# Kernel optimization log

Hardware: AMD Instinct MI355X
Metric: run time of the kernel (lower is better)

## Reference

```python
import jax, jax.numpy as jnp
import numpy as np

CURVS = (-1.0, 0.0, 1.0, -0.5)
N, E, B = 50000, 800000, 128
IN, HID, OUT, GHID = 128, 128, 128, 32
K = len(CURVS)
TAU_MIN, TAU_MAX = 0.05, 10.0
EPS = 1e-15


def _vnorm(x):
    return jnp.maximum(jnp.linalg.norm(x, axis=-1, keepdims=True), EPS)


def tan_k(x, k):
    if k > 0:
        sk = np.sqrt(k)
        return jnp.tan(x * sk) / sk
    if k < 0:
        sk = np.sqrt(-k)
        return jnp.tanh(x * sk) / sk
    return x


def artan_k(x, k):
    if k > 0:
        sk = np.sqrt(k)
        return jnp.arctan(x * sk) / sk
    if k < 0:
        sk = np.sqrt(-k)
        return jnp.arctanh(jnp.clip(x * sk, -1.0 + 1e-7, 1.0 - 1e-7)) / sk
    return x


def project(x, k):
    # clip inside Poincare ball for k<0; identity otherwise (geoopt Stereographic.projx)
    if k < 0:
        maxn = (1.0 - 1e-5) / np.sqrt(-k)
        n = _vnorm(x)
        return jnp.where(n > maxn, x * (maxn / n), x)
    return x


def expmap0(u, k):
    n = _vnorm(u)
    return project(tan_k(n, k) * u / n, k)


def logmap0(y, k):
    n = _vnorm(y)
    return artan_k(n, k) * y / n


def mobius_add(x, y, k):
    x2 = jnp.sum(x * x, -1, keepdims=True)
    y2 = jnp.sum(y * y, -1, keepdims=True)
    xy = jnp.sum(x * y, -1, keepdims=True)
    num = (1.0 - 2.0 * k * xy - k * y2) * x + (1.0 + k * x2) * y
    den = jnp.maximum(1.0 - 2.0 * k * xy + k * k * x2 * y2, 1e-15)
    return project(num / den, k)


def mobius_matvec(W, x, k):
    mx = x @ W.T
    if k == 0:
        return mx
    xn = _vnorm(x)
    mxn = _vnorm(mx)
    res = tan_k(mxn / xn * artan_k(xn, k), k) * mx / mxn
    res = jnp.where(jnp.sum(jnp.abs(mx), -1, keepdims=True) == 0.0, 0.0, res)
    return project(res, k)


def dist(x, y, k):
    return 2.0 * artan_k(_vnorm(mobius_add(-x, y, k)), k)[..., 0]


def setup_inputs():
    key = jax.random.key(0)
    ks = jax.random.split(key, 12)
    x = jax.random.normal(ks[0], (N, IN), jnp.float32)
    edge_index = jax.random.randint(ks[1], (2, E), 0, N)
    batch = jnp.sort(jax.random.randint(ks[2], (N,), 0, B))
    s1 = float(np.sqrt(2.0 / (IN + HID)))
    s2 = float(np.sqrt(2.0 / (HID + OUT)))
    sg1 = float(np.sqrt(2.0 / (IN + GHID)))
    sg2 = float(np.sqrt(2.0 / (GHID + OUT)))
    raw0 = float(np.log(np.expm1(1.0 - TAU_MIN)))
    return {
        "x": x,
        "edge_index": edge_index,
        "batch": batch,
        "expert_w1": jax.random.normal(ks[3], (K, HID, IN), jnp.float32) * s1,
        "expert_b1": jnp.zeros((K, HID), jnp.float32),
        "expert_w2": jax.random.normal(ks[4], (K, OUT, HID), jnp.float32) * s2,
        "expert_b2": jnp.zeros((K, OUT), jnp.float32),
        "gate_w1": jax.random.normal(ks[5], (GHID, IN), jnp.float32) * sg1,
        "gate_b1": jnp.zeros((GHID,), jnp.float32),
        "gate_w2": jax.random.normal(ks[6], (OUT, GHID), jnp.float32) * sg2,
        "gate_b2": jnp.zeros((OUT,), jnp.float32),
        "gate_u": jax.random.normal(ks[7], (K, OUT), jnp.float32) * 0.02,
        "tau_raw": jnp.full((K,), raw0, jnp.float32),
    }


def _graph_norm(edge_index):
    loops = jnp.arange(N)
    row = jnp.concatenate([edge_index[0], loops])
    col = jnp.concatenate([edge_index[1], loops])
    deg = jax.ops.segment_sum(jnp.ones(E + N, jnp.float32), col, num_segments=N)
    dinv = deg ** -0.5  # deg >= 1 due to self loops
    return row, col, dinv[row] * dinv[col]


def _kappa_conv(xm, W, b, row, col, enorm, k):
    h = mobius_matvec(W, xm, k)
    bias_pt = expmap0(b[None, :], k)  # proju at origin is identity
    h = mobius_add(h, bias_pt, k)
    t = logmap0(h, k)  # [N, out]
    agg = jax.ops.segment_sum(enorm[:, None] * t[row], col, num_segments=N)
    return expmap0(agg, k)


def reference(x, edge_index, batch, expert_w1, expert_b1, expert_w2, expert_b2,
              gate_w1, gate_b1, gate_w2, gate_b2, gate_u, tau_raw):
    x = x.astype(jnp.float32)
    row, col, enorm = _graph_norm(edge_index)
    counts = jnp.maximum(
        jax.ops.segment_sum(jnp.ones(N, jnp.float32), batch, num_segments=B), 1.0)[:, None]

    # --- Riemannian experts ---
    embs = []
    for i, kv in enumerate(CURVS):
        xm = expmap0(x, kv)  # manifold init (proju at origin = identity)
        xm = _kappa_conv(xm, expert_w1[i], expert_b1[i], row, col, enorm, kv)
        xm = _kappa_conv(xm, expert_w2[i], expert_b2[i], row, col, enorm, kv)
        z = logmap0(xm, kv)
        embs.append(jax.ops.segment_sum(z, batch, num_segments=B) / counts)
    features = jnp.concatenate(embs, axis=-1)  # [B, K*OUT]

    # --- Euclidean gating encoder (GCN) ---
    def gcn(h, W, b):
        m = (h @ W.T)
        out = jax.ops.segment_sum(enorm[:, None] * m[row], col, num_segments=N) + b
        return jax.nn.relu(out)

    g = gcn(x, gate_w1, gate_b1)
    g = gcn(g, gate_w2, gate_b2)
    hgate = jax.ops.segment_sum(g, batch, num_segments=B) / counts  # [B, OUT]

    # --- Geometric distance gate ---
    tau = jnp.clip(jax.nn.softplus(tau_raw) + TAU_MIN, TAU_MIN, TAU_MAX)
    dists = []
    for i, kv in enumerate(CURVS):
        zk = expmap0(hgate, kv)
        yk = expmap0(gate_u[i][None, :], kv)
        dists.append(dist(zk, yk, kv))
    dists = jnp.stack(dists, axis=-1)  # [B, K]
    weights = jax.nn.softmax(-dists / tau[None, :], axis=-1)

    scaled = features * jnp.repeat(weights, OUT, axis=1)
    return scaled, weights, dists, tau
```

## Files before the change

### kernel.cpp

```cpp
#include <hip/hip_runtime.h>
#include <math.h>

#define NN 50000
#define EE 800000
#define ETOT (EE + NN)
#define BB 128
#define DIM 128
#define GHID 32
#define CHUNK 128
#define NCHUNK ((ETOT + CHUNK - 1) / CHUNK)
#define SCB 196

typedef _Float16 f16;
typedef _Float16 f16x2 __attribute__((ext_vector_type(2)));
typedef _Float16 f16x8 __attribute__((ext_vector_type(8)));
typedef float f32x4 __attribute__((ext_vector_type(4)));

struct CurvPack {
  float k[4], sk[4], mx[4], thr2[4];
};

__device__ __forceinline__ float wsum64(float v) {
#pragma unroll
  for (int m = 32; m; m >>= 1) v += __shfl_xor(v, m, 64);
  return v;
}

__device__ __forceinline__ float tan_k_d(float x, float kv, float sk) {
  if (kv > 0.f) return tanf(x * sk) / sk;
  if (kv < 0.f) return tanhf(x * sk) / sk;
  return x;
}

__device__ __forceinline__ float artan_k_d(float x, float kv, float sk) {
  if (kv > 0.f) return atanf(x * sk) / sk;
  if (kv < 0.f) {
    float t = x * sk;
    t = fminf(fmaxf(t, -1.f + 1e-7f), 1.f - 1e-7f);
    return atanhf(t) / sk;
  }
  return x;
}

__device__ __forceinline__ float proj_scale_d(float n, float kv, float maxn) {
  if (kv < 0.f && n > maxn) return maxn / n;
  return 1.f;
}

__global__ void k_init(float* __restrict__ deg, int n) {
  int i = blockIdx.x * 256 + threadIdx.x;
  if (i < n) deg[i] = 1.0f;
}

__global__ void k_counts(const int* __restrict__ batch, int* __restrict__ boff,
                         float* __restrict__ counts, int n) {
  int b = threadIdx.x;
  if (b <= 128) {
    int lo = 0, hi = n;
    while (lo < hi) {
      int mid = (lo + hi) >> 1;
      if (batch[mid] < b) lo = mid + 1; else hi = mid;
    }
    boff[b] = lo;
  }
  __syncthreads();
  if (b < 128) counts[b] = (float)(boff[b + 1] - boff[b]);
}

__global__ void k_deg(const int* __restrict__ ei, float* __restrict__ deg, int e) {
  int i = blockIdx.x * 256 + threadIdx.x;
  if (i < e) atomicAdd(&deg[ei[e + i]], 1.0f);
}

__global__ void k_dinv(float* __restrict__ deg, int* __restrict__ ideg, int n) {
  int i = blockIdx.x * 256 + threadIdx.x;
  if (i < n) {
    float d = deg[i];
    ideg[i] = (int)(d + 0.5f);
    deg[i] = 1.0f / sqrtf(d);
  }
}

__global__ void k_scanA(const int* __restrict__ ideg, int* __restrict__ bsum, int n) {
  __shared__ int ls[4];
  int i = blockIdx.x * 256 + threadIdx.x;
  int v = (i < n) ? ideg[i] : 0;
#pragma unroll
  for (int m = 1; m < 64; m <<= 1) v += __shfl_xor(v, m, 64);
  if ((threadIdx.x & 63) == 0) ls[threadIdx.x >> 6] = v;
  __syncthreads();
  if (threadIdx.x == 0) bsum[blockIdx.x] = ls[0] + ls[1] + ls[2] + ls[3];
}

__global__ void k_scanB(int* __restrict__ bsum, int nb) {
  __shared__ int wsh[4];
  int tid = threadIdx.x;
  int lane = tid & 63, w = tid >> 6;
  int v = (tid < nb) ? bsum[tid] : 0;
  int x = v;
#pragma unroll
  for (int o = 1; o < 64; o <<= 1) {
    int t = __shfl_up(x, o, 64);
    if (lane >= o) x += t;
  }
  if (lane == 63) wsh[w] = x;
  __syncthreads();
  int add = 0;
  for (int k2 = 0; k2 < w; k2++) add += wsh[k2];
  if (tid < nb) bsum[tid] = add + x - v;
}

__global__ void k_scanC(const int* __restrict__ ideg, const int* __restrict__ bsum,
                        int* __restrict__ off, int* __restrict__ cursor, int n) {
  __shared__ int wsh[4];
  int i = blockIdx.x * 256 + threadIdx.x;
  int lane = threadIdx.x & 63, w = threadIdx.x >> 6;
  int v = (i < n) ? ideg[i] : 0;
  int x = v;
#pragma unroll
  for (int o = 1; o < 64; o <<= 1) {
    int t = __shfl_up(x, o, 64);
    if (lane >= o) x += t;
  }
  if (lane == 63) wsh[w] = x;
  __syncthreads();
  int add = bsum[blockIdx.x];
  for (int k2 = 0; k2 < w; k2++) add += wsh[k2];
  int excl = add + x - v;
  if (i < n) {
    off[i] = excl;
    cursor[i] = excl;
  }
  if (i == n - 1) off[n] = excl + v;
}

__global__ void k_bnodes(const int* __restrict__ off, int* __restrict__ bnode, int nchunk,
                         int n) {
  int g = blockIdx.x * 256 + threadIdx.x;
  if (g >= nchunk) return;
  int e0 = g * CHUNK;
  int lo = 0, hi = n;
  while (hi - lo > 1) {
    int mid = (lo + hi) >> 1;
    if (off[mid] <= e0) lo = mid; else hi = mid;
  }
  bnode[g] = lo;
}

__global__ void k_bslot(const int* __restrict__ bnode, int* __restrict__ bslot, int nchunk) {
  int g = blockIdx.x * 256 + threadIdx.x;
  if (g >= nchunk) return;
  int v = bnode[g];
  int lo = 0, hi = g;
  while (lo < hi) {
    int mid = (lo + hi) >> 1;
    if (bnode[mid] < v) lo = mid + 1; else hi = mid;
  }
  bslot[g] = lo;
}

__device__ __forceinline__ bool span_head(const int* bnode, const int* bslot, const int* off,
                                          int g, int& nd) {
  if (bslot[g] != g) return false;
  nd = bnode[g];
  int s = off[nd], e = off[nd + 1];
  return (s / CHUNK) != ((e - 1) / CHUNK);
}

__global__ void k_zeroc(const int* __restrict__ bnode, const int* __restrict__ bslot,
                        const int* __restrict__ off, float* __restrict__ aggc, int nchunk) {
  int g = blockIdx.x * 4 + (threadIdx.x >> 6);
  int lane = threadIdx.x & 63;
  if (g >= nchunk) return;
  int nd;
  if (!span_head(bnode, bslot, off, g, nd)) return;
  float2 z = make_float2(0.f, 0.f);
#pragma unroll
  for (int i = 0; i < 5; i++) ((float2*)aggc)[(size_t)g * 320 + i * 64 + lane] = z;
}

__global__ void k_place(const int* __restrict__ ei, const float* __restrict__ dinv,
                        int* __restrict__ cursor, int2* __restrict__ esw, int e, int n) {
  int i = blockIdx.x * 256 + threadIdx.x;
  int et = e + n;
  if (i >= et) return;
  int r_, c_;
  if (i < e) {
    r_ = ei[i];
    c_ = ei[e + i];
  } else {
    r_ = i - e;
    c_ = i - e;
  }
  int p = atomicAdd(&cursor[c_], 1);
  esw[p] = make_int2(r_, __float_as_int(dinv[r_] * dinv[c_]));
}

__global__ void k_biaspt_all(const float* __restrict__ eb1, const float* __restrict__ eb2,
                             float* __restrict__ biasb, CurvPack cp) {
  __shared__ float l2[2];
  int blk = blockIdx.x;
  int ex = blk >> 1, layer = blk & 1;
  float kv = cp.k[ex], sk = cp.sk[ex], maxn = cp.mx[ex];
  const float* b = (layer ? eb2 : eb1) + ex * 128;
  float* outb = biasb + blk * 132;
  int j = threadIdx.x;
  float v = b[j];
  float n2 = wsum64(v * v);
  if ((j & 63) == 0) l2[j >> 6] = n2;
  __syncthreads();
  n2 = l2[0] + l2[1];
  float nraw = sqrtf(n2);
  float nnv = fmaxf(nraw, 1e-15f);
  float tk = tan_k_d(nnv, kv, sk);
  float s = tk / nnv;
  float pn = fmaxf(fabsf(tk) * (nraw / nnv), 1e-15f);
  float ps = proj_scale_d(pn, kv, maxn);
  float bp = ps * s * v;
  outb[j] = bp;
  float y2v = wsum64(bp * bp);
  __syncthreads();
  if ((j & 63) == 0) l2[j >> 6] = y2v;
  __syncthreads();
  if (j == 0) outb[128] = l2[0] + l2[1];
}

__global__ void k_w2h(const float* __restrict__ ew1, const float* __restrict__ ew2,
                      f16* __restrict__ whi, f16* __restrict__ wlo) {
  int i = blockIdx.x * 256 + threadIdx.x;
  if (i >= 8 * 16384) return;
  int slot = i >> 14;
  int r = i & 16383;
  int ex = slot >> 1, layer = slot & 1;
  float w = (layer ? ew2 : ew1)[ex * 16384 + r];
  f16 h = (f16)w;
  whi[i] = h;
  wlo[i] = (f16)(w - (float)h);
}

__global__ __launch_bounds__(256) void k_matmfma(
    const float* __restrict__ A, int astr, int aoffPerEx,
    const f16* __restrict__ whiB, const f16* __restrict__ wloB,
    const float* __restrict__ biasB, int layer, f16* __restrict__ tout, int n,
    CurvPack cp) {
  __shared__ float red[3][16][4];
  __shared__ float redT[16][4];
  __shared__ float nAs[16], nCs[16], nL[16];
  int ex = blockIdx.y;
  float kv = cp.k[ex], sk = cp.sk[ex], maxn = cp.mx[ex];
  const f16* whi = whiB + (size_t)(ex * 2 + layer) * 16384;
  const f16* wlo = wloB + (size_t)(ex * 2 + layer) * 16384;
  const float* biasb = biasB + (ex * 2 + layer) * 132;

  int tid = threadIdx.x;
  int w = tid >> 6;
  int lane = tid & 63;
  int col = lane & 15;
  int quad = lane >> 4;
  int n0w = blockIdx.x * 16;
  if (n0w >= n) return;

  int anodec = min(n0w + col, n - 1);
  const float* arow = A + (size_t)anodec * astr + ex * aoffPerEx;
  int jt0 = w * 2;

  f32x4 acc[2];
  acc[0] = (f32x4){0.f, 0.f, 0.f, 0.f};
  acc[1] = (f32x4){0.f, 0.f, 0.f, 0.f};
  float a_n2 = 0.f;

#pragma unroll
  for (int kc = 0; kc < 4; kc++) {
    int kb = kc * 32 + quad * 8;
    float4 a0 = *(const float4*)(arow + kb);
    float4 a1 = *(const float4*)(arow + kb + 4);
    float av[8] = {a0.x, a0.y, a0.z, a0.w, a1.x, a1.y, a1.z, a1.w};
    f16x8 Ah, Al;
// ... 94 lines not shown
  }
  __syncthreads();

  if (tid < 16) {
    float t0f = redT[tid][0] + redT[tid][1] + redT[tid][2] + redT[tid][3];
    float nraw = sqrtf(t0f);
    float ps2 = proj_scale_d(fmaxf(nraw, 1e-15f), kv, maxn);
    float nh = fmaxf(ps2 * nraw, 1e-15f);
    nL[tid] = artan_k_d(nh, kv, sk) / nh * ps2;
  }
  __syncthreads();

#pragma unroll
  for (int r = 0; r < 4; r++) {
    int idx = quad * 4 + r;
    int gnode = n0w + idx;
    if (gnode >= n) continue;
    float Asc = nAs[idx], Cs = nCs[idx], L = nL[idx];
    f16* trow = tout + (size_t)gnode * 512;
#pragma unroll
    for (int j2 = 0; j2 < 2; j2++) {
      float v = fmaf(Asc, acc[j2][r], Cs * bpj[j2]);
      int d = (jt0 + j2) * 16 + col;
      trow[(d >> 1) * 8 + ex * 2 + (d & 1)] = (f16)(L * v);
    }
  }
}

template <int MODE>
__global__ __launch_bounds__(256) void k_aggF(
    const int2* __restrict__ esw, const int* __restrict__ off,
    const int* __restrict__ bnode, const int* __restrict__ bslot,
    const int* __restrict__ batch, const f16x8* __restrict__ t,
    const float* __restrict__ gm1, const f16x2* __restrict__ tg,
    float* __restrict__ agg1, float* __restrict__ aggc,
    float* __restrict__ g1, float* __restrict__ feats,
    const float* __restrict__ gbias, float* __restrict__ hgate,
    int etot, CurvPack cp) {
  int gw = blockIdx.x * 4 + (threadIdx.x >> 6);
  int lane = threadIdx.x & 63;
  int e0 = gw * CHUNK;
  if (e0 >= etot) return;
  int e1 = min(e0 + CHUNK, etot);
  int lane31 = lane & 31;
  int bnHead = bnode[gw];
  int slotA = bslot[gw];
  int slotB = ((gw + 1) * CHUNK < etot) ? bslot[gw + 1] : slotA;

  int2 mv0 = esw[min(e0 + lane, etot - 1)];
  int2 mv1 = esw[min(e0 + 64 + lane, etot - 1)];
  int offv = off[min(bnHead + lane, NN)];
  int batchv = 0;
  if (MODE == 1) batchv = batch[min(bnHead + lane, NN - 1)];

  int cur = bnHead;
  int runStart = __builtin_amdgcn_readlane(offv, 0);
  int eend = __builtin_amdgcn_readlane(offv, 1);

  auto nextOff = [&](int c1) -> int {
    int rel = c1 - bnHead;
    if (rel < 64) return __builtin_amdgcn_readlane(offv, rel);
    return off[c1];
  };
  auto curBatch = [&](int c) -> int {
    int rel = c - bnHead;
    if (rel < 64) return __builtin_amdgcn_readlane(batchv, rel);
    return batch[c];
  };

  float ax[4], ay[4], pax[4], pay[4];
#pragma unroll
  for (int e = 0; e < 4; e++) ax[e] = ay[e] = pax[e] = pay[e] = 0.f;
  float gx = 0.f, gy = 0.f, pgx = 0.f, pgy = 0.f;
  int bcur = (MODE == 1) ? __builtin_amdgcn_readlane(batchv, 0) : 0;
  float bbx, bby = 0.f;
  if (MODE == 0) {
    bbx = gbias[lane31];
  } else {
    float2 bb = ((const float2*)gbias)[lane];
    bbx = bb.x;
    bby = bb.y;
  }

  auto flushInterior = [&]() {
#pragma unroll
    for (int e = 0; e < 4; e++) {
      if (MODE == 0) {
        ((float2*)agg1)[(size_t)cur * 256 + e * 64 + lane] = make_float2(ax[e], ay[e]);
      } else {
        float n2 = wsum64(fmaf(ax[e], ax[e], ay[e] * ay[e]));
        if (n2 <= cp.thr2[e]) {
          pax[e] += ax[e];
          pay[e] += ay[e];
        } else {
          float nraw = sqrtf(n2);
          float nnv = fmaxf(nraw, 1e-15f);
          float tk = tan_k_d(nnv, cp.k[e], cp.sk[e]);
          float s = tk / nnv;
          float pn = fmaxf(fabsf(tk) * (nraw / nnv), 1e-15f);
          float ps = proj_scale_d(pn, cp.k[e], cp.mx[e]);
          s *= ps;
          float nh = fmaxf(pn * ps, 1e-15f);
          float sc = artan_k_d(nh, cp.k[e], cp.sk[e]) / nh * s;
          pax[e] = fmaf(sc, ax[e], pax[e]);
          pay[e] = fmaf(sc, ay[e], pay[e]);
        }
      }
    }
    if (MODE == 0) {
      if (lane < 32) g1[(size_t)cur * 32 + lane] = fmaxf(gx + bbx, 0.f);
    } else {
      pgx += fmaxf(gx + bbx, 0.f);
      pgy += fmaxf(gy + bby, 0.f);
    }
  };
  auto flushBoundary = [&]() {
    int slot = (cur == bnHead) ? slotA : slotB;
    float* dp = aggc + (size_t)slot * 640;
#pragma unroll
    for (int e = 0; e < 4; e++) {
      atomicAdd(dp + e * 128 + lane * 2, ax[e]);
      atomicAdd(dp + e * 128 + lane * 2 + 1, ay[e]);
    }
    if (MODE == 0) {
      if (lane < 32) atomicAdd(dp + 512 + lane, gx);
    } else {
      atomicAdd(dp + 512 + lane * 2, gx);
      atomicAdd(dp + 512 + lane * 2 + 1, gy);
    }
  };
  auto flushPool = [&]() {
#pragma unroll
    for (int e = 0; e < 4; e++) {
      float* fp = &feats[(size_t)bcur * 512 + e * 128 + lane * 2];
      atomicAdd(fp, pax[e]);
      atomicAdd(fp + 1, pay[e]);
    }
    float* hp = &hgate[(size_t)bcur * 128 + lane * 2];
    atomicAdd(hp, pgx);
    atomicAdd(hp + 1, pgy);
  };

  f16x8 rv[8];
  float gf[8];
  f16x2 gh[8];

#pragma unroll
  for (int b = 0; b < CHUNK / 8; b++) {
    int jb = e0 + b * 8;
    if (jb < e1) {
      const int2 mvsel = (b < 8) ? mv0 : mv1;
#pragma unroll
      for (int q = 0; q < 8; q++) {
        int s = __builtin_amdgcn_readlane(mvsel.x, (b & 7) * 8 + q);
        rv[q] = t[(size_t)s * 64 + lane];
        if (MODE == 0) gf[q] = gm1[(size_t)s * 32 + lane31];
        else gh[q] = tg[(size_t)s * 64 + lane];
      }
#pragma unroll
      for (int q = 0; q < 8; q++) {
        if (jb + q == eend) {
          if (runStart >= e0) flushInterior(); else flushBoundary();
#pragma unroll
          for (int e = 0; e < 4; e++) ax[e] = ay[e] = 0.f;
          gx = gy = 0.f;
          runStart = jb + q;
          cur++;
          eend = nextOff(cur + 1);
          if (MODE == 1) {
            int nbt = curBatch(cur);
            if (nbt != bcur) {
              flushPool();
#pragma unroll
              for (int e = 0; e < 4; e++) pax[e] = pay[e] = 0.f;
              pgx = pgy = 0.f;
              bcur = nbt;
            }
          }
        }
        float w = __int_as_float(__builtin_amdgcn_readlane(mvsel.y, (b & 7) * 8 + q));
#pragma unroll
        for (int e = 0; e < 4; e++) {
          ax[e] = fmaf(w, (float)rv[q][2 * e], ax[e]);
          ay[e] = fmaf(w, (float)rv[q][2 * e + 1], ay[e]);
        }
        if (MODE == 0) {
          gx = fmaf(w, gf[q], gx);
        } else {
          gx = fmaf(w, (float)gh[q][0], gx);
          gy = fmaf(w, (float)gh[q][1], gy);
        }
      }
    }
  }
  if (runStart >= e0 && eend <= e1) flushInterior(); else flushBoundary();
  if (MODE == 1) flushPool();
}

__global__ void k_fix1(const int* __restrict__ bnode, const int* __restrict__ bslot,
                       const int* __restrict__ off, const float* __restrict__ aggc,
                       float* __restrict__ agg1, float* __restrict__ g1,
                       const float* __restrict__ gb1, int nchunk) {
  int g = blockIdx.x * 4 + (threadIdx.x >> 6);
  int lane = threadIdx.x & 63;
  if (g >= nchunk) return;
  int nd;
  if (!span_head(bnode, bslot, off, g, nd)) return;
  const float* sp = aggc + (size_t)g * 640;
#pragma unroll
  for (int e = 0; e < 4; e++) {
    float2 v = ((const float2*)sp)[e * 64 + lane];
    ((float2*)agg1)[(size_t)nd * 256 + e * 64 + lane] = v;
  }
  if (lane < 32) g1[(size_t)nd * 32 + lane] = fmaxf(sp[512 + lane] + gb1[lane], 0.f);
}

__global__ void k_fix2(const int* __restrict__ bnode, const int* __restrict__ bslot,
                       const int* __restrict__ off, const float* __restrict__ aggc,
                       const int* __restrict__ batch, float* __restrict__ feats,
                       const float* __restrict__ gb2, float* __restrict__ hgate,
                       int nchunk, CurvPack cp) {
  int g = blockIdx.x * 4 + (threadIdx.x >> 6);
  int lane = threadIdx.x & 63;
  if (g >= nchunk) return;
  int nd;
  if (!span_head(bnode, bslot, off, g, nd)) return;
  int b = batch[nd];
  const float* sp = aggc + (size_t)g * 640;
#pragma unroll
  for (int e = 0; e < 4; e++) {
    float2 v = ((const float2*)sp)[e * 64 + lane];
    float n2 = wsum64(fmaf(v.x, v.x, v.y * v.y));
    float nraw = sqrtf(n2);
    float nnv = fmaxf(nraw, 1e-15f);
    float tk = tan_k_d(nnv, cp.k[e], cp.sk[e]);
    float s = tk / nnv;
    float pn = fmaxf(fabsf(tk) * (nraw / nnv), 1e-15f);
    float ps = proj_scale_d(pn, cp.k[e], cp.mx[e]);
    s *= ps;
    float nh = fmaxf(pn * ps, 1e-15f);
    float sc = artan_k_d(nh, cp.k[e], cp.sk[e]) / nh * s;
    float* fp = &feats[(size_t)b * 512 + e * 128 + lane * 2];
    atomicAdd(fp, sc * v.x);
    atomicAdd(fp + 1, sc * v.y);
  }
  float2 gv = ((const float2*)(sp + 512))[lane];
  float2 bb = ((const float2*)gb2)[lane];
  float* hp = &hgate[(size_t)b * 128 + lane * 2];
  atomicAdd(hp, fmaxf(gv.x + bb.x, 0.f));
  atomicAdd(hp + 1, fmaxf(gv.y + bb.y, 0.f));
}

__global__ __launch_bounds__(256) void k_gate1(const float* __restrict__ x,
                                               const float* __restrict__ gw1,
                                               float* __restrict__ m1, int n) {
  __shared__ float xT[64][68];
  __shared__ float Wt[64][36];
  int tid = threadIdx.x;
  int n0 = blockIdx.x * 64;
  int c = tid & 7, r = tid >> 3;
  float acc[2][4];
#pragma unroll
  for (int i = 0; i < 2; i++)
#pragma unroll
    for (int jj = 0; jj < 4; jj++) acc[i][jj] = 0.f;

  for (int kc = 0; kc < 2; kc++) {
    if (kc) __syncthreads();
#pragma unroll
    for (int it = 0; it < 8; it++) {
      int u = tid + it * 256;
      int j = u >> 6, kd = u & 63;
      Wt[kd][j] = gw1[j * 128 + kc * 64 + kd];
    }
#pragma unroll
    for (int it = 0; it < 4; it++) {
      int u = tid + it * 256;
      int node = u >> 4, c4 = u & 15;
      float4 v = make_float4(0.f, 0.f, 0.f, 0.f);
      if (n0 + node < n) v = ((const float4*)x)[(size_t)(n0 + node) * 32 + kc * 16 + c4];
      xT[4 * c4 + 0][node] = v.x;
      xT[4 * c4 + 1][node] = v.y;
      xT[4 * c4 + 2][node] = v.z;
      xT[4 * c4 + 3][node] = v.w;
    }
    __syncthreads();
#pragma unroll 8
    for (int kd = 0; kd < 64; kd++) {
      float2 av = *(const float2*)&xT[kd][r * 2];
      float4 bv = *(const float4*)&Wt[kd][c * 4];
      float a[2] = {av.x, av.y};
      float bbv[4] = {bv.x, bv.y, bv.z, bv.w};
#pragma unroll
      for (int i = 0; i < 2; i++)
#pragma unroll
        for (int jj = 0; jj < 4; jj++) acc[i][jj] = fmaf(a[i], bbv[jj], acc[i][jj]);
    }
  }
#pragma unroll
  for (int i = 0; i < 2; i++) {
    int node = n0 + r * 2 + i;
    if (node >= n) continue;
    ((float4*)m1)[(size_t)node * 8 + c] = make_float4(acc[i][0], acc[i][1], acc[i][2], acc[i][3]);
  }
}

__global__ __launch_bounds__(256) void k_gate2(const float* __restrict__ g1,
                                               const float* __restrict__ gw2,
                                               f16* __restrict__ m2, int n) {
  __shared__ float xT[32][68];
  __shared__ float Wt[32][132];
  int tid = threadIdx.x;
  int n0 = blockIdx.x * 64;
  int c = tid & 15, r = tid >> 4;
  float acc[4][8];
#pragma unroll
  for (int i = 0; i < 4; i++)
#pragma unroll
    for (int jj = 0; jj < 8; jj++) acc[i][jj] = 0.f;

#pragma unroll
  for (int it = 0; it < 16; it++) {
    int u = tid + it * 256;
    int j = u >> 5, kd = u & 31;
    Wt[kd][j] = gw2[j * 32 + kd];
  }
#pragma unroll
  for (int it = 0; it < 2; it++) {
    int u = tid + it * 256;
    int node = u >> 3, c4 = u & 7;
    float4 v = make_float4(0.f, 0.f, 0.f, 0.f);
    if (n0 + node < n) v = ((const float4*)g1)[(size_t)(n0 + node) * 8 + c4];
    xT[4 * c4 + 0][node] = v.x;
    xT[4 * c4 + 1][node] = v.y;
    xT[4 * c4 + 2][node] = v.z;
    xT[4 * c4 + 3][node] = v.w;
  }
  __syncthreads();
#pragma unroll 8
  for (int kd = 0; kd < 32; kd++) {
    float4 av = *(const float4*)&xT[kd][r * 4];
    float4 b0 = *(const float4*)&Wt[kd][c * 8];
    float4 b1 = *(const float4*)&Wt[kd][c * 8 + 4];
    float a[4] = {av.x, av.y, av.z, av.w};
    float bbv[8] = {b0.x, b0.y, b0.z, b0.w, b1.x, b1.y, b1.z, b1.w};
#pragma unroll
    for (int i = 0; i < 4; i++)
#pragma unroll
      for (int jj = 0; jj < 8; jj++) acc[i][jj] = fmaf(a[i], bbv[jj], acc[i][jj]);
  }
#pragma unroll
  for (int i = 0; i < 4; i++) {
    int node = n0 + r * 4 + i;
    if (node >= n) continue;
    f16x8 hv;
#pragma unroll
    for (int jj = 0; jj < 8; jj++) hv[jj] = (f16)acc[i][jj];
    *((f16x8*)(m2 + (size_t)node * 128) + c) = hv;
  }
}

__global__ __launch_bounds__(128) void k_final(const float* __restrict__ feats,
                                               const float* __restrict__ hgate,
                                               const float* __restrict__ counts,
                                               const float* __restrict__ gate_u,
                                               const float* __restrict__ tau_raw,
                                               float* __restrict__ out, CurvPack cp) {
  __shared__ float l2[2];
  int b = blockIdx.x;
  int j = threadIdx.x;
  float cnt = fmaxf(counts[b], 1.f);
  float hg = hgate[(size_t)b * 128 + j] / cnt;

  auto bsum = [&](float v) -> float {
    v = wsum64(v);
    __syncthreads();
    if ((j & 63) == 0) l2[j >> 6] = v;
    __syncthreads();
    return l2[0] + l2[1];
  };

  float nhg2 = bsum(hg * hg);
  float nhgraw = sqrtf(nhg2);
  float nhg = fmaxf(nhgraw, 1e-15f);

  float d[4], tau[4];
#pragma unroll
  for (int i = 0; i < 4; i++) {
    float kv = cp.k[i], sk = cp.sk[i], mxn = cp.mx[i];
    float tk = tan_k_d(nhg, kv, sk);
    float s = tk / nhg;
    float pn = fmaxf(fabsf(tk) * (nhgraw / nhg), 1e-15f);
// ... 60 lines not shown
                              void* d_out, int out_size, void* d_ws, size_t ws_size,
                              hipStream_t stream) {
  const float* x = (const float*)d_in[0];
  const int* ei = (const int*)d_in[1];
  const int* batch = (const int*)d_in[2];
  const float* ew1 = (const float*)d_in[3];
  const float* eb1 = (const float*)d_in[4];
  const float* ew2 = (const float*)d_in[5];
  const float* eb2 = (const float*)d_in[6];
  const float* gw1 = (const float*)d_in[7];
  const float* gb1 = (const float*)d_in[8];
  const float* gw2 = (const float*)d_in[9];
  const float* gb2 = (const float*)d_in[10];
  const float* gu = (const float*)d_in[11];
  const float* traw = (const float*)d_in[12];
  float* out = (float*)d_out;

  const int N = NN, E = EE, ET = ETOT, B = BB;

  float* ws = (float*)d_ws;
  size_t o = 0;
  f16* t4 = (f16*)ws;       o += (size_t)N * 256;
  float* agg1 = ws + o;     o += (size_t)N * 512;
  float* aggc = ws + o;     o += (size_t)NCHUNK * 640;
  float* deg = ws + o;      o += N;
  float* counts = ws + o;   o += 256;
  float* feats = ws + o;    o += (size_t)B * 512;
  float* hg = ws + o;       o += (size_t)B * 128;
  float* biasb = ws + o;    o += 8 * 132;
  f16* whi = (f16*)(ws + o);    o += 8 * 16384 / 2;
  f16* wlo = (f16*)(ws + o);    o += 8 * 16384 / 2;
  float* m1 = ws + o;       o += (size_t)N * 32;
  float* g1 = ws + o;       o += (size_t)N * 32;
  f16* tg = (f16*)(ws + o); o += (size_t)N * 64;
  int* ideg = (int*)(ws + o);   o += N;
  int* csroff = (int*)(ws + o); o += N + 8;
  int* cursor = (int*)(ws + o); o += N;
  int* boff = (int*)(ws + o);   o += 136;
  int* bsum = (int*)(ws + o);   o += 256;
  int* bnode = (int*)(ws + o);  o += NCHUNK + 8;
  int* bslot = (int*)(ws + o);  o += NCHUNK + 8;
  int2* esw = (int2*)(ws + o);  o += (size_t)2 * ET;

  hipMemsetAsync(counts, 0, (256 + (size_t)B * 512 + (size_t)B * 128) * sizeof(float), stream);

  const double curvs[4] = {-1.0, 0.0, 1.0, -0.5};
  CurvPack cp;
  for (int i = 0; i < 4; i++) {
    double kd = curvs[i];
    double skd = sqrt(fabs(kd));
    cp.k[i] = (float)kd;
    cp.sk[i] = (float)skd;
    cp.mx[i] = (kd < 0) ? (float)((1.0 - 1e-5) / skd) : 3.0e38f;
    if (kd < 0) {
      double thr = 6.0 / skd;
      cp.thr2[i] = (float)(thr * thr);
    } else if (kd > 0) {
      double thr = 1.5 / skd;
      cp.thr2[i] = (float)(thr * thr);
    } else {
      cp.thr2[i] = 3.0e38f;
    }
  }

  k_init<<<(N + 255) / 256, 256, 0, stream>>>(deg, N);
  k_counts<<<1, 256, 0, stream>>>(batch, boff, counts, N);
  k_deg<<<(E + 255) / 256, 256, 0, stream>>>(ei, deg, E);
  k_dinv<<<(N + 255) / 256, 256, 0, stream>>>(deg, ideg, N);
  k_scanA<<<SCB, 256, 0, stream>>>(ideg, bsum, N);
  k_scanB<<<1, 256, 0, stream>>>(bsum, SCB);
  k_scanC<<<SCB, 256, 0, stream>>>(ideg, bsum, csroff, cursor, N);
  k_bnodes<<<(NCHUNK + 255) / 256, 256, 0, stream>>>(csroff, bnode, NCHUNK, N);
  k_bslot<<<(NCHUNK + 255) / 256, 256, 0, stream>>>(bnode, bslot, NCHUNK);
  k_place<<<(ET + 255) / 256, 256, 0, stream>>>(ei, deg, cursor, esw, E, N);
  k_biaspt_all<<<8, 128, 0, stream>>>(eb1, eb2, biasb, cp);
  k_w2h<<<512, 256, 0, stream>>>(ew1, ew2, whi, wlo);
  k_gate1<<<(N + 63) / 64, 256, 0, stream>>>(x, gw1, m1, N);

  const int aggBlocks = (NCHUNK + 3) / 4;
  dim3 mfmaGrid((N + 15) / 16, 4);

  k_matmfma<<<mfmaGrid, 256, 0, stream>>>(x, 128, 0, whi, wlo, biasb, 0, t4, N, cp);
  k_zeroc<<<aggBlocks, 256, 0, stream>>>(bnode, bslot, csroff, aggc, NCHUNK);
  k_aggF<0><<<aggBlocks, 256, 0, stream>>>(esw, csroff, bnode, bslot, batch,
                                           (const f16x8*)t4, m1, nullptr, agg1, aggc, g1,
                                           nullptr, gb1, nullptr, ET, cp);
  k_fix1<<<aggBlocks, 256, 0, stream>>>(bnode, bslot, csroff, aggc, agg1, g1, gb1, NCHUNK);
  k_gate2<<<(N + 63) / 64, 256, 0, stream>>>(g1, gw2, tg, N);

  k_matmfma<<<mfmaGrid, 256, 0, stream>>>(agg1, 512, 128, whi, wlo, biasb, 1, t4, N, cp);
  k_zeroc<<<aggBlocks, 256, 0, stream>>>(bnode, bslot, csroff, aggc, NCHUNK);
  k_aggF<1><<<aggBlocks, 256, 0, stream>>>(esw, csroff, bnode, bslot, batch,
                                           (const f16x8*)t4, nullptr, (const f16x2*)tg,
                                           nullptr, aggc, nullptr, feats, gb2, hg, ET, cp);
  k_fix2<<<aggBlocks, 256, 0, stream>>>(bnode, bslot, csroff, aggc, batch, feats, gb2, hg,
                                        NCHUNK, cp);

  k_final<<<B, 128, 0, stream>>>(feats, hg, counts, gu, traw, out, cp);

  (void)in_sizes; (void)n_in; (void)out_size; (void)ws_size;
}
```

Baseline: 963.3 us.

## Merge setup kernels and fold second gate GEMM into aggregation

Several small setup kernels (degree count, batch offsets, bias projection, weight splitting, first gate GEMM) are merged into one multi-role launch, and the edge placement, chunk-node search and slot computation are merged into another. Zeroing of the boundary accumulators moves into an extra grid row of the MFMA kernel. The second gate layer is reordered to aggregate the 32-wide hidden features first and then multiply by gw2 per node inside the aggregation and fix-up kernels. This removes the k_gate2 kernel and its 128-wide fp16 intermediate, and means gathers read 32 floats instead of 128 halves. The cost is extra per-node matvec work and larger shared memory in the aggregation kernel.

```diff
diff --git a/kernel.cpp b/kernel.cpp
--- a/kernel.cpp
+++ b/kernel.cpp
@@ -11,6 +11,13 @@
 #define NCHUNK ((ETOT + CHUNK - 1) / CHUNK)
 #define SCB 196
 
+#define DEGB 3125
+#define G1B 782
+#define W2HB 512
+#define MEGA0B (DEGB + G1B + W2HB + 1 + 8)
+#define PLACEB 3321
+#define BNB ((NCHUNK + 255) / 256)
+
 typedef _Float16 f16;
 typedef _Float16 f16x2 __attribute__((ext_vector_type(2)));
 typedef _Float16 f16x8 __attribute__((ext_vector_type(8)));
@@ -47,35 +54,139 @@
   return 1.f;
 }
 
-__global__ void k_init(float* __restrict__ deg, int n) {
-  int i = blockIdx.x * 256 + threadIdx.x;
-  if (i < n) deg[i] = 1.0f;
-}
-
-__global__ void k_counts(const int* __restrict__ batch, int* __restrict__ boff,
-                         float* __restrict__ counts, int n) {
-  int b = threadIdx.x;
-  if (b <= 128) {
-    int lo = 0, hi = n;
-    while (lo < hi) {
-      int mid = (lo + hi) >> 1;
-      if (batch[mid] < b) lo = mid + 1; else hi = mid;
-    }
-    boff[b] = lo;
-  }
-  __syncthreads();
-  if (b < 128) counts[b] = (float)(boff[b + 1] - boff[b]);
-}
-
-__global__ void k_deg(const int* __restrict__ ei, float* __restrict__ deg, int e) {
-  int i = blockIdx.x * 256 + threadIdx.x;
-  if (i < e) atomicAdd(&deg[ei[e + i]], 1.0f);
+__global__ __launch_bounds__(256) void k_mega0(
+    const int* __restrict__ ei, float* __restrict__ deg, const int* __restrict__ batch,
+    int* __restrict__ boff, float* __restrict__ counts, const float* __restrict__ eb1,
+    const float* __restrict__ eb2, float* __restrict__ biasb, const float* __restrict__ ew1,
+    const float* __restrict__ ew2, f16* __restrict__ whi, f16* __restrict__ wlo,
+    const float* __restrict__ x, const float* __restrict__ gw1, float* __restrict__ m1,
+    CurvPack cp) {
+  __shared__ float smem[64 * 68 + 64 * 36];
+  int bx = blockIdx.x;
+  int tid = threadIdx.x;
+
+  if (bx < DEGB) {
+    int i = bx * 256 + tid;
+    if (i < EE) atomicAdd(&deg[ei[EE + i]], 1.0f);
+    return;
+  }
+  bx -= DEGB;
+
+  if (bx < G1B) {
+    float(*xT)[68] = (float(*)[68])smem;
+    float(*Wt)[36] = (float(*)[36])(smem + 64 * 68);
+    int n0 = bx * 64;
+    int c = tid & 7, r = tid >> 3;
+    float acc[2][4];
+#pragma unroll
+    for (int i = 0; i < 2; i++)
+#pragma unroll
+      for (int jj = 0; jj < 4; jj++) acc[i][jj] = 0.f;
+    for (int kc = 0; kc < 2; kc++) {
+      if (kc) __syncthreads();
+#pragma unroll
+      for (int it = 0; it < 8; it++) {
+        int u = tid + it * 256;
+        int j = u >> 6, kd = u & 63;
+        Wt[kd][j] = gw1[j * 128 + kc * 64 + kd];
+      }
+#pragma unroll
+      for (int it = 0; it < 4; it++) {
+        int u = tid + it * 256;
+        int node = u >> 4, c4 = u & 15;
+        float4 v = make_float4(0.f, 0.f, 0.f, 0.f);
+        if (n0 + node < NN) v = ((const float4*)x)[(size_t)(n0 + node) * 32 + kc * 16 + c4];
+        xT[4 * c4 + 0][node] = v.x;
+        xT[4 * c4 + 1][node] = v.y;
+        xT[4 * c4 + 2][node] = v.z;
+        xT[4 * c4 + 3][node] = v.w;
+      }
+      __syncthreads();
+#pragma unroll 8
+      for (int kd = 0; kd < 64; kd++) {
+        float2 av = *(const float2*)&xT[kd][r * 2];
+        float4 bv = *(const float4*)&Wt[kd][c * 4];
+        float a[2] = {av.x, av.y};
+        float bbv[4] = {bv.x, bv.y, bv.z, bv.w};
+#pragma unroll
+        for (int i = 0; i < 2; i++)
+#pragma unroll
+          for (int jj = 0; jj < 4; jj++) acc[i][jj] = fmaf(a[i], bbv[jj], acc[i][jj]);
+      }
+    }
+#pragma unroll
+    for (int i = 0; i < 2; i++) {
+      int node = n0 + r * 2 + i;
+      if (node >= NN) continue;
+      ((float4*)m1)[(size_t)node * 8 + c] =
+          make_float4(acc[i][0], acc[i][1], acc[i][2], acc[i][3]);
+    }
+    return;
+  }
+  bx -= G1B;
+
+  if (bx < W2HB) {
+    int i = bx * 256 + tid;
+    if (i >= 8 * 16384) return;
+    int slot = i >> 14;
+    int r = i & 16383;
+    int ex = slot >> 1, layer = slot & 1;
+    float w = (layer ? ew2 : ew1)[ex * 16384 + r];
+    f16 h = (f16)w;
+    whi[i] = h;
+    wlo[i] = (f16)(w - (float)h);
+    return;
+  }
+  bx -= W2HB;
+
+  if (bx == 0) {
+    int b = tid;
+    if (b <= 128) {
+      int lo = 0, hi = NN;
+      while (lo < hi) {
+        int mid = (lo + hi) >> 1;
+        if (batch[mid] < b) lo = mid + 1; else hi = mid;
+      }
+      boff[b] = lo;
+    }
+    __syncthreads();
+    if (b < 128) counts[b] = (float)(boff[b + 1] - boff[b]);
+    return;
+  }
+  bx -= 1;
+
+  {
+    float* l2 = smem;
+    int ex = bx >> 1, layer = bx & 1;
+    float kv = cp.k[ex], sk = cp.sk[ex], maxn = cp.mx[ex];
+    const float* b = (layer ? eb2 : eb1) + ex * 128;
+    float* outb = biasb + bx * 132;
+    int j = tid;
+    float v = (j < 128) ? b[j] : 0.f;
+    float n2 = wsum64(v * v);
+    if ((j & 63) == 0) l2[j >> 6] = n2;
+    __syncthreads();
+    n2 = l2[0] + l2[1];
+    float nraw = sqrtf(n2);
+    float nnv = fmaxf(nraw, 1e-15f);
+    float tk = tan_k_d(nnv, kv, sk);
+    float s = tk / nnv;
+    float pn = fmaxf(fabsf(tk) * (nraw / nnv), 1e-15f);
+    float ps = proj_scale_d(pn, kv, maxn);
+    float bp = ps * s * v;
+    if (j < 128) outb[j] = bp;
+    float y2v = wsum64(bp * bp);
+    __syncthreads();
+    if ((j & 63) == 0) l2[j >> 6] = y2v;
+    __syncthreads();
+    if (j == 0) outb[128] = l2[0] + l2[1];
+  }
 }
 
 __global__ void k_dinv(float* __restrict__ deg, int* __restrict__ ideg, int n) {
   int i = blockIdx.x * 256 + threadIdx.x;
   if (i < n) {
-    float d = deg[i];
+    float d = deg[i] + 1.0f;
     ideg[i] = (int)(d + 0.5f);
     deg[i] = 1.0f / sqrtf(d);
   }
@@ -134,29 +245,37 @@
   if (i == n - 1) off[n] = excl + v;
 }
 
-__global__ void k_bnodes(const int* __restrict__ off, int* __restrict__ bnode, int nchunk,
-                         int n) {
-  int g = blockIdx.x * 256 + threadIdx.x;
-  if (g >= nchunk) return;
+__global__ void k_megapre(const int* __restrict__ ei, const float* __restrict__ dinv,
+                          int* __restrict__ cursor, int2* __restrict__ esw,
+                          const int* __restrict__ off, int* __restrict__ bnode,
+                          int* __restrict__ bslot) {
+  int bx = blockIdx.x;
+  if (bx < PLACEB) {
+    int i = bx * 256 + threadIdx.x;
+    if (i >= ETOT) return;
+    int r_, c_;
+    if (i < EE) {
+      r_ = ei[i];
+      c_ = ei[EE + i];
+    } else {
+      r_ = i - EE;
+      c_ = i - EE;
+    }
+    int p = atomicAdd(&cursor[c_], 1);
+    esw[p] = make_int2(r_, __float_as_int(dinv[r_] * dinv[c_]));
+    return;
+  }
+  bx -= PLACEB;
+  int g = bx * 256 + threadIdx.x;
+  if (g >= NCHUNK) return;
   int e0 = g * CHUNK;
-  int lo = 0, hi = n;
+  int lo = 0, hi = NN;
   while (hi - lo > 1) {
     int mid = (lo + hi) >> 1;
     if (off[mid] <= e0) lo = mid; else hi = mid;
   }
   bnode[g] = lo;
-}
-
-__global__ void k_bslot(const int* __restrict__ bnode, int* __restrict__ bslot, int nchunk) {
-  int g = blockIdx.x * 256 + threadIdx.x;
-  if (g >= nchunk) return;
-  int v = bnode[g];
-  int lo = 0, hi = g;
-  while (lo < hi) {
-    int mid = (lo + hi) >> 1;
-    if (bnode[mid] < v) lo = mid + 1; else hi = mid;
-  }
-  bslot[g] = lo;
+  bslot[g] = (off[lo] + CHUNK - 1) / CHUNK;
 }
 
 __device__ __forceinline__ bool span_head(const int* bnode, const int* bslot, const int* off,
@@ -167,82 +286,23 @@
   return (s / CHUNK) != ((e - 1) / CHUNK);
 }
 
-__global__ void k_zeroc(const int* __restrict__ bnode, const int* __restrict__ bslot,
-                        const int* __restrict__ off, float* __restrict__ aggc, int nchunk) {
-  int g = blockIdx.x * 4 + (threadIdx.x >> 6);
-  int lane = threadIdx.x & 63;
-  if (g >= nchunk) return;
-  int nd;
-  if (!span_head(bnode, bslot, off, g, nd)) return;
-  float2 z = make_float2(0.f, 0.f);
-#pragma unroll
-  for (int i = 0; i < 5; i++) ((float2*)aggc)[(size_t)g * 320 + i * 64 + lane] = z;
-}
-
-__global__ void k_place(const int* __restrict__ ei, const float* __restrict__ dinv,
-                        int* __restrict__ cursor, int2* __restrict__ esw, int e, int n) {
-  int i = blockIdx.x * 256 + threadIdx.x;
-  int et = e + n;
-  if (i >= et) return;
-  int r_, c_;
-  if (i < e) {
-    r_ = ei[i];
-    c_ = ei[e + i];
-  } else {
-    r_ = i - e;
-    c_ = i - e;
-  }
-  int p = atomicAdd(&cursor[c_], 1);
-  esw[p] = make_int2(r_, __float_as_int(dinv[r_] * dinv[c_]));
-}
-
-__global__ void k_biaspt_all(const float* __restrict__ eb1, const float* __restrict__ eb2,
-                             float* __restrict__ biasb, CurvPack cp) {
-  __shared__ float l2[2];
-  int blk = blockIdx.x;
-  int ex = blk >> 1, layer = blk & 1;
-  float kv = cp.k[ex], sk = cp.sk[ex], maxn = cp.mx[ex];
-  const float* b = (layer ? eb2 : eb1) + ex * 128;
-  float* outb = biasb + blk * 132;
-  int j = threadIdx.x;
-  float v = b[j];
-  float n2 = wsum64(v * v);
-  if ((j & 63) == 0) l2[j >> 6] = n2;
-  __syncthreads();
-  n2 = l2[0] + l2[1];
-  float nraw = sqrtf(n2);
-  float nnv = fmaxf(nraw, 1e-15f);
-  float tk = tan_k_d(nnv, kv, sk);
-  float s = tk / nnv;
-  float pn = fmaxf(fabsf(tk) * (nraw / nnv), 1e-15f);
-  float ps = proj_scale_d(pn, kv, maxn);
-  float bp = ps * s * v;
-  outb[j] = bp;
-  float y2v = wsum64(bp * bp);
-  __syncthreads();
-  if ((j & 63) == 0) l2[j >> 6] = y2v;
-  __syncthreads();
-  if (j == 0) outb[128] = l2[0] + l2[1];
-}
-
-__global__ void k_w2h(const float* __restrict__ ew1, const float* __restrict__ ew2,
-                      f16* __restrict__ whi, f16* __restrict__ wlo) {
-  int i = blockIdx.x * 256 + threadIdx.x;
-  if (i >= 8 * 16384) return;
-  int slot = i >> 14;
-  int r = i & 16383;
-  int ex = slot >> 1, layer = slot & 1;
-  float w = (layer ? ew2 : ew1)[ex * 16384 + r];
-  f16 h = (f16)w;
-  whi[i] = h;
-  wlo[i] = (f16)(w - (float)h);
-}
-
 __global__ __launch_bounds__(256) void k_matmfma(
     const float* __restrict__ A, int astr, int aoffPerEx,
     const f16* __restrict__ whiB, const f16* __restrict__ wloB,
     const float* __restrict__ biasB, int layer, f16* __restrict__ tout, int n,
-    CurvPack cp) {
+    const int* __restrict__ bnode, const int* __restrict__ bslot,
+    const int* __restrict__ off, float* __restrict__ aggc, CurvPack cp) {
+  if (blockIdx.y == 4) {
+    int g = blockIdx.x * 4 + (threadIdx.x >> 6);
+    int lane = threadIdx.x & 63;
+    if (g >= NCHUNK) return;
+    int nd;
+    if (!span_head(bnode, bslot, off, g, nd)) return;
+    float2 z = make_float2(0.f, 0.f);
+#pragma unroll
+    for (int i = 0; i < 5; i++) ((float2*)aggc)[(size_t)g * 320 + i * 64 + lane] = z;
+    return;
+  }
   __shared__ float red[3][16][4];
   __shared__ float redT[16][4];
   __shared__ float nAs[16], nCs[16], nL[16];
@@ -403,11 +463,19 @@
     const int2* __restrict__ esw, const int* __restrict__ off,
     const int* __restrict__ bnode, const int* __restrict__ bslot,
     const int* __restrict__ batch, const f16x8* __restrict__ t,
-    const float* __restrict__ gm1, const f16x2* __restrict__ tg,
-    float* __restrict__ agg1, float* __restrict__ aggc,
-    float* __restrict__ g1, float* __restrict__ feats,
-    const float* __restrict__ gbias, float* __restrict__ hgate,
-    int etot, CurvPack cp) {
+    const float* __restrict__ gsrc, float* __restrict__ agg1, float* __restrict__ aggc,
+    float* __restrict__ g1out, float* __restrict__ feats,
+    const float* __restrict__ gbias, const float* __restrict__ gw2,
+    float* __restrict__ hgate, int etot, CurvPack cp) {
+  __shared__ float gw2s[(MODE == 1) ? 32 : 1][128];
+  if (MODE == 1) {
+#pragma unroll
+    for (int i2 = 0; i2 < 16; i2++) {
+      int u = threadIdx.x + i2 * 256;
+      gw2s[u >> 7][u & 127] = gw2[(u & 127) * 32 + (u >> 7)];
+    }
+    __syncthreads();
+  }
   int gw = blockIdx.x * 4 + (threadIdx.x >> 6);
   int lane = threadIdx.x & 63;
   int e0 = gw * CHUNK;
@@ -442,7 +510,7 @@
   float ax[4], ay[4], pax[4], pay[4];
 #pragma unroll
   for (int e = 0; e < 4; e++) ax[e] = ay[e] = pax[e] = pay[e] = 0.f;
-  float gx = 0.f, gy = 0.f, pgx = 0.f, pgy = 0.f;
+  float gx = 0.f, pgx = 0.f, pgy = 0.f;
   int bcur = (MODE == 1) ? __builtin_amdgcn_readlane(batchv, 0) : 0;
   float bbx, bby = 0.f;
   if (MODE == 0) {
@@ -479,10 +547,18 @@
       }
     }
     if (MODE == 0) {
-      if (lane < 32) g1[(size_t)cur * 32 + lane] = fmaxf(gx + bbx, 0.f);
+      if (lane < 32) g1out[(size_t)cur * 32 + lane] = fmaxf(gx + bbx, 0.f);
     } else {
-      pgx += fmaxf(gx + bbx, 0.f);
-      pgy += fmaxf(gy + bby, 0.f);
+      float o0 = 0.f, o1 = 0.f;
+#pragma unroll
+      for (int k2 = 0; k2 < 32; k2++) {
+        float agk = __int_as_float(__builtin_amdgcn_readlane(__float_as_int(gx), k2));
+        float2 wv = *(const float2*)&gw2s[k2][lane * 2];
+        o0 = fmaf(agk, wv.x, o0);
+        o1 = fmaf(agk, wv.y, o1);
+      }
+      pgx += fmaxf(o0 + bbx, 0.f);
+      pgy += fmaxf(o1 + bby, 0.f);
     }
   };
   auto flushBoundary = [&]() {
@@ -493,12 +569,7 @@
       atomicAdd(dp + e * 128 + lane * 2, ax[e]);
       atomicAdd(dp + e * 128 + lane * 2 + 1, ay[e]);
     }
-    if (MODE == 0) {
-      if (lane < 32) atomicAdd(dp + 512 + lane, gx);
-    } else {
-      atomicAdd(dp + 512 + lane * 2, gx);
-      atomicAdd(dp + 512 + lane * 2 + 1, gy);
-    }
+    if (lane < 32) atomicAdd(dp + 512 + lane, gx);
   };
   auto flushPool = [&]() {
 #pragma unroll
@@ -514,7 +585,6 @@
 
   f16x8 rv[8];
   float gf[8];
-  f16x2 gh[8];
 
 #pragma unroll
   for (int b = 0; b < CHUNK / 8; b++) {
@@ -525,8 +595,7 @@
       for (int q = 0; q < 8; q++) {
         int s = __builtin_amdgcn_readlane(mvsel.x, (b & 7) * 8 + q);
         rv[q] = t[(size_t)s * 64 + lane];
-        if (MODE == 0) gf[q] = gm1[(size_t)s * 32 + lane31];
-        else gh[q] = tg[(size_t)s * 64 + lane];
+        gf[q] = gsrc[(size_t)s * 32 + lane31];
       }
 #pragma unroll
       for (int q = 0; q < 8; q++) {
@@ -534,7 +603,7 @@
           if (runStart >= e0) flushInterior(); else flushBoundary();
 #pragma unroll
           for (int e = 0; e < 4; e++) ax[e] = ay[e] = 0.f;
-          gx = gy = 0.f;
+          gx = 0.f;
           runStart = jb + q;
           cur++;
           eend = nextOff(cur + 1);
@@ -555,12 +624,7 @@
           ax[e] = fmaf(w, (float)rv[q][2 * e], ax[e]);
           ay[e] = fmaf(w, (float)rv[q][2 * e + 1], ay[e]);
         }
-        if (MODE == 0) {
-          gx = fmaf(w, gf[q], gx);
-        } else {
-          gx = fmaf(w, (float)gh[q][0], gx);
-          gy = fmaf(w, (float)gh[q][1], gy);
-        }
+        gx = fmaf(w, gf[q], gx);
       }
     }
   }
@@ -589,8 +653,8 @@
 __global__ void k_fix2(const int* __restrict__ bnode, const int* __restrict__ bslot,
                        const int* __restrict__ off, const float* __restrict__ aggc,
                        const int* __restrict__ batch, float* __restrict__ feats,
-                       const float* __restrict__ gb2, float* __restrict__ hgate,
-                       int nchunk, CurvPack cp) {
+                       const float* __restrict__ gb2, const float* __restrict__ gw2,
+                       float* __restrict__ hgate, int nchunk, CurvPack cp) {
   int g = blockIdx.x * 4 + (threadIdx.x >> 6);
   int lane = threadIdx.x & 63;
   if (g >= nchunk) return;
@@ -615,120 +679,17 @@
     atomicAdd(fp, sc * v.x);
     atomicAdd(fp + 1, sc * v.y);
   }
-  float2 gv = ((const float2*)(sp + 512))[lane];
   float2 bb = ((const float2*)gb2)[lane];
+  float o0 = 0.f, o1 = 0.f;
+#pragma unroll 8
+  for (int k2 = 0; k2 < 32; k2++) {
+    float agk = sp[512 + k2];
+    o0 = fmaf(agk, gw2[(2 * lane) * 32 + k2], o0);
+    o1 = fmaf(agk, gw2[(2 * lane + 1) * 32 + k2], o1);
+  }
   float* hp = &hgate[(size_t)b * 128 + lane * 2];
-  atomicAdd(hp, fmaxf(gv.x + bb.x, 0.f));
-  atomicAdd(hp + 1, fmaxf(gv.y + bb.y, 0.f));
-}
-
-__global__ __launch_bounds__(256) void k_gate1(const float* __restrict__ x,
-                                               const float* __restrict__ gw1,
-                                               float* __restrict__ m1, int n) {
-  __shared__ float xT[64][68];
-  __shared__ float Wt[64][36];
-  int tid = threadIdx.x;
-  int n0 = blockIdx.x * 64;
-  int c = tid & 7, r = tid >> 3;
-  float acc[2][4];
-#pragma unroll
-  for (int i = 0; i < 2; i++)
-#pragma unroll
-    for (int jj = 0; jj < 4; jj++) acc[i][jj] = 0.f;
-
-  for (int kc = 0; kc < 2; kc++) {
-    if (kc) __syncthreads();
-#pragma unroll
-    for (int it = 0; it < 8; it++) {
-      int u = tid + it * 256;
-      int j = u >> 6, kd = u & 63;
-      Wt[kd][j] = gw1[j * 128 + kc * 64 + kd];
-    }
-#pragma unroll
-    for (int it = 0; it < 4; it++) {
-      int u = tid + it * 256;
-      int node = u >> 4, c4 = u & 15;
-      float4 v = make_float4(0.f, 0.f, 0.f, 0.f);
-      if (n0 + node < n) v = ((const float4*)x)[(size_t)(n0 + node) * 32 + kc * 16 + c4];
-      xT[4 * c4 + 0][node] = v.x;
-      xT[4 * c4 + 1][node] = v.y;
-      xT[4 * c4 + 2][node] = v.z;
-      xT[4 * c4 + 3][node] = v.w;
-    }
-    __syncthreads();
-#pragma unroll 8
-    for (int kd = 0; kd < 64; kd++) {
-      float2 av = *(const float2*)&xT[kd][r * 2];
-      float4 bv = *(const float4*)&Wt[kd][c * 4];
-      float a[2] = {av.x, av.y};
-      float bbv[4] = {bv.x, bv.y, bv.z, bv.w};
-#pragma unroll
-      for (int i = 0; i < 2; i++)
-#pragma unroll
-        for (int jj = 0; jj < 4; jj++) acc[i][jj] = fmaf(a[i], bbv[jj], acc[i][jj]);
-    }
-  }
-#pragma unroll
-  for (int i = 0; i < 2; i++) {
-    int node = n0 + r * 2 + i;
-    if (node >= n) continue;
-    ((float4*)m1)[(size_t)node * 8 + c] = make_float4(acc[i][0], acc[i][1], acc[i][2], acc[i][3]);
-  }
-}
-
-__global__ __launch_bounds__(256) void k_gate2(const float* __restrict__ g1,
-                                               const float* __restrict__ gw2,
-                                               f16* __restrict__ m2, int n) {
-  __shared__ float xT[32][68];
-  __shared__ float Wt[32][132];
-  int tid = threadIdx.x;
-  int n0 = blockIdx.x * 64;
-  int c = tid & 15, r = tid >> 4;
-  float acc[4][8];
-#pragma unroll
-  for (int i = 0; i < 4; i++)
-#pragma unroll
-    for (int jj = 0; jj < 8; jj++) acc[i][jj] = 0.f;
-
-#pragma unroll
-  for (int it = 0; it < 16; it++) {
-    int u = tid + it * 256;
-    int j = u >> 5, kd = u & 31;
-    Wt[kd][j] = gw2[j * 32 + kd];
-  }
-#pragma unroll
-  for (int it = 0; it < 2; it++) {
-    int u = tid + it * 256;
-    int node = u >> 3, c4 = u & 7;
-    float4 v = make_float4(0.f, 0.f, 0.f, 0.f);
-    if (n0 + node < n) v = ((const float4*)g1)[(size_t)(n0 + node) * 8 + c4];
-    xT[4 * c4 + 0][node] = v.x;
-    xT[4 * c4 + 1][node] = v.y;
-    xT[4 * c4 + 2][node] = v.z;
-    xT[4 * c4 + 3][node] = v.w;
-  }
-  __syncthreads();
-#pragma unroll 8
-  for (int kd = 0; kd < 32; kd++) {
-    float4 av = *(const float4*)&xT[kd][r * 4];
-    float4 b0 = *(const float4*)&Wt[kd][c * 8];
-    float4 b1 = *(const float4*)&Wt[kd][c * 8 + 4];
-    float a[4] = {av.x, av.y, av.z, av.w};
-    float bbv[8] = {b0.x, b0.y, b0.z, b0.w, b1.x, b1.y, b1.z, b1.w};
-#pragma unroll
-    for (int i = 0; i < 4; i++)
-#pragma unroll
-      for (int jj = 0; jj < 8; jj++) acc[i][jj] = fmaf(a[i], bbv[jj], acc[i][jj]);
-  }
-#pragma unroll
-  for (int i = 0; i < 4; i++) {
-    int node = n0 + r * 4 + i;
-    if (node >= n) continue;
-    f16x8 hv;
-#pragma unroll
-    for (int jj = 0; jj < 8; jj++) hv[jj] = (f16)acc[i][jj];
-    *((f16x8*)(m2 + (size_t)node * 128) + c) = hv;
-  }
+  atomicAdd(hp, fmaxf(o0 + bb.x, 0.f));
+  atomicAdd(hp + 1, fmaxf(o1 + bb.y, 0.f));
 }
 
 __global__ __launch_bounds__(128) void k_final(const float* __restrict__ feats,
@@ -855,7 +816,6 @@
   f16* wlo = (f16*)(ws + o);    o += 8 * 16384 / 2;
   float* m1 = ws + o;       o += (size_t)N * 32;
   float* g1 = ws + o;       o += (size_t)N * 32;
-  f16* tg = (f16*)(ws + o); o += (size_t)N * 64;
   int* ideg = (int*)(ws + o);   o += N;
   int* csroff = (int*)(ws + o); o += N + 8;
   int* cursor = (int*)(ws + o); o += N;
@@ -865,7 +825,8 @@
   int* bslot = (int*)(ws + o);  o += NCHUNK + 8;
   int2* esw = (int2*)(ws + o);  o += (size_t)2 * ET;
 
-  hipMemsetAsync(counts, 0, (256 + (size_t)B * 512 + (size_t)B * 128) * sizeof(float), stream);
+  hipMemsetAsync(deg, 0, ((size_t)N + 256 + (size_t)B * 512 + (size_t)B * 128) * sizeof(float),
+                 stream);
 
   const double curvs[4] = {-1.0, 0.0, 1.0, -0.5};
   CurvPack cp;
@@ -886,37 +847,30 @@
     }
   }
 
-  k_init<<<(N + 255) / 256, 256, 0, stream>>>(deg, N);
-  k_counts<<<1, 256, 0, stream>>>(batch, boff, counts, N);
-  k_deg<<<(E + 255) / 256, 256, 0, stream>>>(ei, deg, E);
-  k_dinv<<<(N + 255) / 256, 256, 0, stream>>>(deg, ideg, N);
+  k_mega0<<<MEGA0B, 256, 0, stream>>>(ei, deg, batch, boff, counts, eb1, eb2, biasb, ew1, ew2,
+                                      whi, wlo, x, gw1, m1, cp);
+  k_dinv<<<SCB, 256, 0, stream>>>(deg, ideg, N);
   k_scanA<<<SCB, 256, 0, stream>>>(ideg, bsum, N);
   k_scanB<<<1, 256, 0, stream>>>(bsum, SCB);
   k_scanC<<<SCB, 256, 0, stream>>>(ideg, bsum, csroff, cursor, N);
-  k_bnodes<<<(NCHUNK + 255) / 256, 256, 0, stream>>>(csroff, bnode, NCHUNK, N);
-  k_bslot<<<(NCHUNK + 255) / 256, 256, 0, stream>>>(bnode, bslot, NCHUNK);
-  k_place<<<(ET + 255) / 256, 256, 0, stream>>>(ei, deg, cursor, esw, E, N);
-  k_biaspt_all<<<8, 128, 0, stream>>>(eb1, eb2, biasb, cp);
-  k_w2h<<<512, 256, 0, stream>>>(ew1, ew2, whi, wlo);
-  k_gate1<<<(N + 63) / 64, 256, 0, stream>>>(x, gw1, m1, N);
+  k_megapre<<<PLACEB + BNB, 256, 0, stream>>>(ei, deg, cursor, esw, csroff, bnode, bslot);
 
   const int aggBlocks = (NCHUNK + 3) / 4;
-  dim3 mfmaGrid((N + 15) / 16, 4);
-
-  k_matmfma<<<mfmaGrid, 256, 0, stream>>>(x, 128, 0, whi, wlo, biasb, 0, t4, N, cp);
-  k_zeroc<<<aggBlocks, 256, 0, stream>>>(bnode, bslot, csroff, aggc, NCHUNK);
-  k_aggF<0><<<aggBlocks, 256, 0, stream>>>(esw, csroff, bnode, bslot, batch,
-                                           (const f16x8*)t4, m1, nullptr, agg1, aggc, g1,
-                                           nullptr, gb1, nullptr, ET, cp);
+  dim3 mfmaGrid((N + 15) / 16, 5);
+
+  k_matmfma<<<mfmaGrid, 256, 0, stream>>>(x, 128, 0, whi, wlo, biasb, 0, t4, N, bnode, bslot,
+                                          csroff, aggc, cp);
+  k_aggF<0><<<aggBlocks, 256, 0, stream>>>(esw, csroff, bnode, bslot, batch, (const f16x8*)t4,
+                                           m1, agg1, aggc, g1, nullptr, gb1, nullptr, nullptr,
+                                           ET, cp);
   k_fix1<<<aggBlocks, 256, 0, stream>>>(bnode, bslot, csroff, aggc, agg1, g1, gb1, NCHUNK);
-  k_gate2<<<(N + 63) / 64, 256, 0, stream>>>(g1, gw2, tg, N);
-
-  k_matmfma<<<mfmaGrid, 256, 0, stream>>>(agg1, 512, 128, whi, wlo, biasb, 1, t4, N, cp);
-  k_zeroc<<<aggBlocks, 256, 0, stream>>>(bnode, bslot, csroff, aggc, NCHUNK);
-  k_aggF<1><<<aggBlocks, 256, 0, stream>>>(esw, csroff, bnode, bslot, batch,
-                                           (const f16x8*)t4, nullptr, (const f16x2*)tg,
-                                           nullptr, aggc, nullptr, feats, gb2, hg, ET, cp);
-  k_fix2<<<aggBlocks, 256, 0, stream>>>(bnode, bslot, csroff, aggc, batch, feats, gb2, hg,
+
+  k_matmfma<<<mfmaGrid, 256, 0, stream>>>(agg1, 512, 128, whi, wlo, biasb, 1, t4, N, bnode,
+                                          bslot, csroff, aggc, cp);
+  k_aggF<1><<<aggBlocks, 256, 0, stream>>>(esw, csroff, bnode, bslot, batch, (const f16x8*)t4,
+                                           g1, nullptr, aggc, nullptr, feats, gb2, gw2, hg, ET,
+                                           cp);
+  k_fix2<<<aggBlocks, 256, 0, stream>>>(bnode, bslot, csroff, aggc, batch, feats, gb2, gw2, hg,
                                         NCHUNK, cp);
 
   k_final<<<B, 128, 0, stream>>>(feats, hg, counts, gu, traw, out, cp);
```

Result: faster. 911.6 us (-5.4%).
